# Performance work log

Hardware: AMD Instinct MI355X
Metric: run time of the kernel (lower is better)

## Reference

```python
import jax, jax.numpy as jnp
import numpy as np

NUM_QUBITS = 4
NUM_LAYERS = 3
B = 16384


def ry(t):
    # t: scalar or [B] -> [2,2] or [B,2,2] complex64
    c = jnp.cos(t / 2)
    s = jnp.sin(t / 2)
    return jnp.stack([jnp.stack([c, -s], -1), jnp.stack([s, c], -1)], -2).astype(jnp.complex64)


def rz(t):
    e = jnp.exp(-0.5j * t.astype(jnp.complex64))
    z = jnp.zeros_like(e)
    return jnp.stack([jnp.stack([e, z], -1), jnp.stack([z, jnp.conj(e)], -1)], -2)


def apply_gate(psi, G, wire):
    # psi: [B,2,2,2,2]; G: [2,2] (shared) or [B,2,2] (per-sample)
    ax = 1 + wire
    psi = jnp.moveaxis(psi, ax, -1)
    if G.ndim == 3:
        psi = jnp.einsum('b...j,bij->b...i', psi, G)
    else:
        psi = jnp.einsum('...j,ij->...i', psi, G)
    return jnp.moveaxis(psi, -1, ax)


def cnot(psi, c, t):
    ca, ta = 1 + c, 1 + t
    p0 = jnp.take(psi, 0, axis=ca)
    p1 = jnp.take(psi, 1, axis=ca)
    p1 = jnp.flip(p1, axis=ta - (1 if ta > ca else 0))
    return jnp.stack([p0, p1], axis=ca)


def quantum_layer(inputs, qw):
    # inputs: [B,4] angles; qw: [3,4,2] circuit weights -> [B,4] PauliZ expvals
    b = inputs.shape[0]
    psi = jnp.zeros((b, 2, 2, 2, 2), jnp.complex64).at[:, 0, 0, 0, 0].set(1.0)
    for w in range(NUM_QUBITS):
        psi = apply_gate(psi, ry(inputs[:, w]), w)
    for l in range(NUM_LAYERS):
        for q in range(NUM_QUBITS):
            psi = apply_gate(psi, ry(qw[l, q, 0]), q)
            psi = apply_gate(psi, rz(qw[l, q, 1]), q)
        for q in range(NUM_QUBITS - 1):
            psi = cnot(psi, q, q + 1)
        psi = cnot(psi, NUM_QUBITS - 1, 0)
    pr = jnp.real(psi * jnp.conj(psi))  # [B,2,2,2,2]
    signs = jnp.array([1.0, -1.0], jnp.float32)
    outs = []
    for w in range(NUM_QUBITS):
        shp = [1, 1, 1, 1, 1]
        shp[1 + w] = 2
        outs.append(jnp.sum(pr * signs.reshape(shp), axis=(1, 2, 3, 4)))
    return jnp.stack(outs, axis=1).astype(jnp.float32)


def setup_inputs() -> dict:
    key = jax.random.key(0)
    ks = jax.random.split(key, 10)
    x = jax.random.normal(ks[0], (B, 1280), jnp.float32)
    W1 = jax.random.normal(ks[1], (1280, 64), jnp.float32) * 0.03
    b1 = jnp.zeros((64,), jnp.float32)
    W2 = jax.random.normal(ks[2], (64, 4), jnp.float32) * 0.12
    b2 = jnp.zeros((4,), jnp.float32)
    qw = jax.random.normal(ks[3], (NUM_LAYERS, NUM_QUBITS, 2), jnp.float32) * 0.1
    Wc1 = jax.random.normal(ks[4], (8, 16), jnp.float32) * 0.35
    bc1 = jnp.zeros((16,), jnp.float32)
    Wc2 = jax.random.normal(ks[5], (16, 1), jnp.float32) * 0.25
    bc2 = jnp.zeros((1,), jnp.float32)
    return {"x": x, "W1": W1, "b1": b1, "W2": W2, "b2": b2, "qw": qw,
            "Wc1": Wc1, "bc1": bc1, "Wc2": Wc2, "bc2": bc2}


def reference(x, W1, b1, W2, b2, qw, Wc1, bc1, Wc2, bc2):
    # reducer: 1280 -> 64 -> 4 with tanh (dropout inactive in eval)
    h = jax.nn.relu(x @ W1 + b1)
    reduced = jnp.tanh(h @ W2 + b2)  # [B,4]
    quantum_out = quantum_layer(reduced, qw)  # [B,4]
    combined = jnp.concatenate([reduced, quantum_out], axis=1)  # [B,8]
    logits = jax.nn.relu(combined @ Wc1 + bc1) @ Wc2 + bc2  # [B,1]
    return logits
```

## Files before the change

kernel.cpp:

```cpp
#include <hip/hip_runtime.h>
#include <math.h>

typedef __attribute__((ext_vector_type(4))) float f32x4;
typedef __attribute__((ext_vector_type(8))) short s16x8;

__device__ __forceinline__ short f2bf_rne(float f) {
  unsigned u = __float_as_uint(f);
  unsigned r = u + 0x7FFFu + ((u >> 16) & 1u);
  return (short)(r >> 16);
}
__device__ __forceinline__ float bf2f(short b) {
  return __uint_as_float(((unsigned)(unsigned short)b) << 16);
}

#define WAIT_VMCNT(N) asm volatile("s_waitcnt vmcnt(" #N ")" ::: "memory")
#define BAR()         __builtin_amdgcn_s_barrier()
#define CFENCE()      asm volatile("" ::: "memory")
#define SCHEDB()      __builtin_amdgcn_sched_barrier(0)

__device__ __forceinline__ void gl_lds16(const void* g, void* l) {
  __builtin_amdgcn_global_load_lds(
      (const __attribute__((address_space(1))) void*)g,
      (__attribute__((address_space(3))) void*)l, 16, 0, 0);
}

#define GLOAD4(D, P) \
  asm volatile("global_load_dwordx4 %0, %1, off" : "=&v"(D) : "v"(P))

__global__ __launch_bounds__(256) void prep_w1(const float* __restrict__ W1,
                                               unsigned short* __restrict__ wf) {
  const int c   = blockIdx.x;
  const int l   = threadIdx.x & 63;
  const int nt  = threadIdx.x >> 6;
  const int kb  = c * 32 + (l >> 4) * 8;
  const int col = nt * 16 + (l & 15);
  s16x8 hi, lo;
#pragma unroll
  for (int j = 0; j < 8; ++j) {
    float f = W1[(kb + j) * 64 + col];
    short h = f2bf_rne(f);
    hi[j] = h;
    lo[j] = f2bf_rne(f - bf2f(h));
  }
  const int slot = (c * 4 + nt) * 2;
  *(s16x8*)(wf + (size_t)(slot * 64 + l) * 8)       = hi;
  *(s16x8*)(wf + (size_t)((slot + 1) * 64 + l) * 8) = lo;
}

#define APPLY_RY(BIT, C, S)                                                  \
  { _Pragma("unroll")                                                        \
    for (int i = 0; i < 16; ++i) {                                           \
      if (!(i & (BIT))) {                                                    \
        const int j = i | (BIT);                                             \
        float ar = re[i], ai = im[i], br = re[j], bi = im[j];                \
        re[i] = fmaf((C), ar, -(S) * br);                                    \
        im[i] = fmaf((C), ai, -(S) * bi);                                    \
        re[j] = fmaf((S), ar, (C) * br);                                     \
        im[j] = fmaf((S), ai, (C) * bi);                                     \
      }                                                                      \
    } }

#define APPLY_RZ(BIT, C, S)                                                  \
  { _Pragma("unroll")                                                        \
    for (int i = 0; i < 16; ++i) {                                           \
      float vr = re[i], vi = im[i];                                          \
      if (!(i & (BIT))) { re[i] = fmaf((C), vr, (S) * vi);                   \
                          im[i] = fmaf((C), vi, -(S) * vr); }                \
      else              { re[i] = fmaf((C), vr, -(S) * vi);                  \
                          im[i] = fmaf((C), vi, (S) * vr); }                 \
    } }

#define APPLY_CNOT(CB, TB)                                                   \
  { _Pragma("unroll")                                                        \
    for (int i = 0; i < 16; ++i) {                                           \
      if ((i & (CB)) && !(i & (TB))) {                                       \
        const int j = i | (TB);                                              \
        float t = re[i]; re[i] = re[j]; re[j] = t;                           \
        t = im[i]; im[i] = im[j]; im[j] = t;                                 \
      }                                                                      \
    } }

__device__ __forceinline__ float qfc_head(
    const float* __restrict__ red, const float* __restrict__ qw,
    const float* __restrict__ Wc1, const float* __restrict__ bc1,
    const float* __restrict__ Wc2, const float* __restrict__ bc2) {
  float re[16], im[16];
#pragma unroll
  for (int i = 0; i < 16; ++i) { re[i] = 0.f; im[i] = 0.f; }
  re[0] = 1.f;
  {
    float s0, c0; sincosf(0.5f * red[0], &s0, &c0); APPLY_RY(8, c0, s0);
    float s1, c1; sincosf(0.5f * red[1], &s1, &c1); APPLY_RY(4, c1, s1);
    float s2, c2; sincosf(0.5f * red[2], &s2, &c2); APPLY_RY(2, c2, s2);
    float s3, c3; sincosf(0.5f * red[3], &s3, &c3); APPLY_RY(1, c3, s3);
  }
  for (int lyr = 0; lyr < 3; ++lyr) {
    const float* ql = qw + lyr * 8;
    { float sn, cn; sincosf(0.5f * ql[0], &sn, &cn); APPLY_RY(8, cn, sn); }
    { float sn, cn; sincosf(0.5f * ql[1], &sn, &cn); APPLY_RZ(8, cn, sn); }
    { float sn, cn; sincosf(0.5f * ql[2], &sn, &cn); APPLY_RY(4, cn, sn); }
    { float sn, cn; sincosf(0.5f * ql[3], &sn, &cn); APPLY_RZ(4, cn, sn); }
    { float sn, cn; sincosf(0.5f * ql[4], &sn, &cn); APPLY_RY(2, cn, sn); }
    { float sn, cn; sincosf(0.5f * ql[5], &sn, &cn); APPLY_RZ(2, cn, sn); }
    { float sn, cn; sincosf(0.5f * ql[6], &sn, &cn); APPLY_RY(1, cn, sn); }
    { float sn, cn; sincosf(0.5f * ql[7], &sn, &cn); APPLY_RZ(1, cn, sn); }
    APPLY_CNOT(8, 4);
    APPLY_CNOT(4, 2);
    APPLY_CNOT(2, 1);
    APPLY_CNOT(1, 8);
  }
  float q0 = 0.f, q1 = 0.f, q2 = 0.f, q3 = 0.f;
#pragma unroll
  for (int i = 0; i < 16; ++i) {
    const float pr = fmaf(re[i], re[i], im[i] * im[i]);
    q0 += (i & 8) ? -pr : pr;
    q1 += (i & 4) ? -pr : pr;
    q2 += (i & 2) ? -pr : pr;
    q3 += (i & 1) ? -pr : pr;
  }
  float logit = bc2[0];
#pragma unroll
  for (int j = 0; j < 16; ++j) {
    float a = bc1[j];
    a = fmaf(red[0], Wc1[j],       a);
    a = fmaf(red[1], Wc1[16 + j],  a);
    a = fmaf(red[2], Wc1[32 + j],  a);
    a = fmaf(red[3], Wc1[48 + j],  a);
    a = fmaf(q0,     Wc1[64 + j],  a);
    a = fmaf(q1,     Wc1[80 + j],  a);
    a = fmaf(q2,     Wc1[96 + j],  a);
    a = fmaf(q3,     Wc1[112 + j], a);
    logit = fmaf(fmaxf(a, 0.f), Wc2[j], logit);
  }
  return logit;
}

__global__ __launch_bounds__(256) void qfc_gemm(
    const float* __restrict__ x,
    const unsigned short* __restrict__ wf,
    float* __restrict__ pw)
{
  __shared__ s16x8 Bs[3][512];

  const int tid  = threadIdx.x;
  const int l    = tid & 63;
  const int wv   = tid >> 6;
  const int bid  = blockIdx.x;
  const int rt   = bid / 5;
  const int kq   = bid - rt * 5;
  const int r0   = rt * 64;
  const int arow = l & 15;
  const int kg   = l >> 4;

  const float* xrow = x + (size_t)(r0 + wv * 16 + arow) * 1280 + kq * 256 + kg * 8;
  const s16x8* wfb = (const s16x8*)wf + (size_t)(kq * 8) * 512 + wv * 128 + l;

  f32x4 acc[4];
#pragma unroll
  for (int nt = 0; nt < 4; ++nt) acc[nt] = (f32x4)(0.f);

  float4 a00, a01, a10, a11, a20, a21;

  gl_lds16(wfb,      &Bs[0][wv * 128]);
  gl_lds16(wfb + 64, &Bs[0][wv * 128 + 64]);
  GLOAD4(a00, xrow);
  GLOAD4(a01, xrow + 4);
  gl_lds16(wfb + 512,      &Bs[1][wv * 128]);
  gl_lds16(wfb + 512 + 64, &Bs[1][wv * 128 + 64]);
  GLOAD4(a10, xrow + 32);
  GLOAD4(a11, xrow + 36);

#define CHUNK(C, AC0, AC1, AN0, AN1)                                          \
  {                                                                           \
    if ((C) < 7) { WAIT_VMCNT(4); } else { WAIT_VMCNT(0); }                   \
    BAR();                                                                    \
    CFENCE();                                                                 \
    SCHEDB();                                                                 \
    if ((C) + 2 < 8) {                                                        \
      const s16x8* bsrc_ = wfb + (size_t)((C) + 2) * 512;                     \
      gl_lds16(bsrc_,      &Bs[((C) + 2) % 3][wv * 128]);                     \
      gl_lds16(bsrc_ + 64, &Bs[((C) + 2) % 3][wv * 128 + 64]);                \
      GLOAD4(AN0, xrow + ((C) + 2) * 32);                                     \
      GLOAD4(AN1, xrow + ((C) + 2) * 32 + 4);                                 \
    }                                                                         \
    SCHEDB();                                                                 \
    float f_[8] = {AC0.x, AC0.y, AC0.z, AC0.w, AC1.x, AC1.y, AC1.z, AC1.w};   \
    s16x8 ah_, al_;                                                           \
    _Pragma("unroll")                                                         \
    for (int j = 0; j < 8; ++j) {                                             \
      short h_ = f2bf_rne(f_[j]);                                             \
      ah_[j] = h_;                                                            \
      al_[j] = (short)(__float_as_uint(f_[j] - bf2f(h_)) >> 16);              \
    }                                                                         \
    _Pragma("unroll")                                                         \
    for (int nt = 0; nt < 4; ++nt) {                                          \
      s16x8 bh_ = Bs[(C) % 3][(nt * 2) * 64 + l];                             \
      s16x8 bl_ = Bs[(C) % 3][(nt * 2 + 1) * 64 + l];                         \
      acc[nt] = __builtin_amdgcn_mfma_f32_16x16x32_bf16(ah_, bh_, acc[nt], 0, 0, 0); \
      acc[nt] = __builtin_amdgcn_mfma_f32_16x16x32_bf16(al_, bh_, acc[nt], 0, 0, 0); \
      acc[nt] = __builtin_amdgcn_mfma_f32_16x16x32_bf16(ah_, bl_, acc[nt], 0, 0, 0); \
    }                                                                         \
  }

  CHUNK(0, a00, a01, a20, a21)
  CHUNK(1, a10, a11, a00, a01)
  CHUNK(2, a20, a21, a10, a11)
  CHUNK(3, a00, a01, a20, a21)
  CHUNK(4, a10, a11, a00, a01)
  CHUNK(5, a20, a21, a10, a11)
  CHUNK(6, a00, a01, a20, a21)
  CHUNK(7, a10, a11, a00, a01)
#undef CHUNK

  float* wsp = pw + (size_t)bid * 4096;
#pragma unroll
  for (int nt = 0; nt < 4; ++nt)
    *(float4*)(wsp + (nt * 16 + arow) * 64 + wv * 16 + kg * 4) =
        make_float4(acc[nt][0], acc[nt][1], acc[nt][2], acc[nt][3]);
}

__global__ __launch_bounds__(256) void qfc_tail(
    const float* __restrict__ pw,
    const float* __restrict__ b1, const float* __restrict__ W2,
    const float* __restrict__ b2, const float* __restrict__ qw,
    const float* __restrict__ Wc1, const float* __restrict__ bc1,
    const float* __restrict__ Wc2, const float* __restrict__ bc2,
    float* __restrict__ out) {
  const int tid = threadIdx.x;
  const int s   = tid >> 2;
  const int cq  = tid & 3;
  const int rt  = blockIdx.x;
  const float* pb = pw + (size_t)rt * 5 * 4096;

  float h4[4] = {0.f, 0.f, 0.f, 0.f};
#pragma unroll
  for (int cc = 0; cc < 16; ++cc) {
    const int c = cq * 16 + cc;
    const int o = c * 64 + s;
    float p = pb[o];
#pragma unroll
    for (int q = 1; q < 5; ++q) p += pb[q * 4096 + o];
    float hv = fmaxf(p + b1[c], 0.f);
    const float4 w2 = *(const float4*)(W2 + c * 4);
    h4[0] = fmaf(hv, w2.x, h4[0]);
    h4[1] = fmaf(hv, w2.y, h4[1]);
    h4[2] = fmaf(hv, w2.z, h4[2]);
    h4[3] = fmaf(hv, w2.w, h4[3]);
  }
#pragma unroll
  for (int k = 0; k < 4; ++k) {
    h4[k] += __shfl_xor(h4[k], 1);
    h4[k] += __shfl_xor(h4[k], 2);
  }

  float red[4];
#pragma unroll
  for (int k = 0; k < 4; ++k) red[k] = tanhf(h4[k] + b2[k]);

  const float logit = qfc_head(red, qw, Wc1, bc1, Wc2, bc2);
  if (cq == 0) out[rt * 64 + s] = logit;
}

#define NKT 20
__global__ __launch_bounds__(256) void qfc_fused(
    const float* __restrict__ x, const float* __restrict__ W1,
    const float* __restrict__ b1, const float* __restrict__ W2,
    const float* __restrict__ b2, const float* __restrict__ qw,
    const float* __restrict__ Wc1, const float* __restrict__ bc1,
    const float* __restrict__ Wc2, const float* __restrict__ bc2,
    float* __restrict__ out) {
  __shared__ float lds[16384];
  const int tid = threadIdx.x;
  const int lane = tid & 63;
  const int wv = tid >> 6;
  const int rg = lane >> 3;
  const int cg = lane & 7;
  const int r0 = blockIdx.x * 64;
  float acc[8][8];
#pragma unroll
  for (int i = 0; i < 8; ++i)
#pragma unroll
    for (int j = 0; j < 8; ++j) acc[i][j] = 0.f;
  const float* xrow = x + (size_t)(r0 + lane) * 1280 + wv * 16;
  const int aBase = wv * 1024;
  const int bBase = 8192 + wv * 1024;
  float4 a_st[4], b_st[4];
  auto issue_loads = [&](int kt) {
    const float* ap = xrow + kt * 64;
#pragma unroll
    for (int i = 0; i < 4; ++i) a_st[i] = *(const float4*)(ap + i * 4);
    const float* bp = W1 + kt * 4096 + wv * 1024 + lane * 4;
#pragma unroll
    for (int i = 0; i < 4; ++i) b_st[i] = *(const float4*)(bp + i * 256);
  };
  auto write_stage = [&](int buf) {
    float* A = &lds[buf * 4096 + aBase];
#pragma unroll
    for (int i = 0; i < 4; ++i) {
      float* p = A + i * 256 + lane;
      p[0] = a_st[i].x; p[64] = a_st[i].y; p[128] = a_st[i].z; p[192] = a_st[i].w;
    }
    float* Bp = &lds[buf * 4096 + bBase + lane * 4];
#pragma unroll
    for (int i = 0; i < 4; ++i) *(float4*)(Bp + i * 256) = b_st[i];
  };
  auto compute_tile = [&](int buf) {
#pragma unroll
    for (int m = 0; m < 16; ++m) {
      const float* Ak = &lds[buf * 4096 + aBase + m * 64];
      const float* Bk = &lds[buf * 4096 + bBase + m * 64];
      const float4 a0 = *(const float4*)(Ak + rg * 8);
      const float4 a1 = *(const float4*)(Ak + rg * 8 + 4);
      const float4 c0 = *(const float4*)(Bk + cg * 8);
      const float4 c1 = *(const float4*)(Bk + cg * 8 + 4);
      const float av[8] = {a0.x, a0.y, a0.z, a0.w, a1.x, a1.y, a1.z, a1.w};
      const float bv[8] = {c0.x, c0.y, c0.z, c0.w, c1.x, c1.y, c1.z, c1.w};
#pragma unroll
      for (int i = 0; i < 8; ++i)
#pragma unroll
        for (int j = 0; j < 8; ++j) acc[i][j] = fmaf(av[i], bv[j], acc[i][j]);
    }
  };
  issue_loads(0);
  write_stage(0);
  for (int kt = 0; kt < NKT; ++kt) {
    const int buf = kt & 1;
    if (kt + 1 < NKT) issue_loads(kt + 1);
    compute_tile(buf);
    if (kt + 1 < NKT) write_stage(buf ^ 1);
  }
  __syncthreads();
#pragma unroll
  for (int j = 0; j < 8; ++j) {
    const int c = cg * 8 + j;
    float* p = &lds[wv * 4096 + c * 64 + rg * 8];
    *(float4*)p = make_float4(acc[0][j], acc[1][j], acc[2][j], acc[3][j]);
    *(float4*)(p + 4) = make_float4(acc[4][j], acc[5][j], acc[6][j], acc[7][j]);
  }
  __syncthreads();
  const int s = tid >> 2;
  const int cq = tid & 3;
  float h4[4] = {0.f, 0.f, 0.f, 0.f};
#pragma unroll
  for (int cc = 0; cc < 16; ++cc) {
    const int c = cq * 16 + cc;
    const int o = c * 64 + s;
    float pp = (lds[o] + lds[4096 + o]) + (lds[8192 + o] + lds[12288 + o]);
    float hv = fmaxf(pp + b1[c], 0.f);
    const float4 w2 = *(const float4*)(W2 + c * 4);
    h4[0] = fmaf(hv, w2.x, h4[0]);
    h4[1] = fmaf(hv, w2.y, h4[1]);
    h4[2] = fmaf(hv, w2.z, h4[2]);
    h4[3] = fmaf(hv, w2.w, h4[3]);
  }
#pragma unroll
  for (int k = 0; k < 4; ++k) {
    h4[k] += __shfl_xor(h4[k], 1);
    h4[k] += __shfl_xor(h4[k], 2);
  }
  float red[4];
#pragma unroll
  for (int k = 0; k < 4; ++k) red[k] = tanhf(h4[k] + b2[k]);
  const float logit = qfc_head(red, qw, Wc1, bc1, Wc2, bc2);
  if (cq == 0) out[r0 + s] = logit;
}

extern "C" void kernel_launch(void* const* d_in, const int* in_sizes, int n_in,
                              void* d_out, int out_size, void* d_ws, size_t ws_size,
                              hipStream_t stream) {
  const float* x   = (const float*)d_in[0];
  const float* W1  = (const float*)d_in[1];
  const float* b1  = (const float*)d_in[2];
  const float* W2  = (const float*)d_in[3];
  const float* b2  = (const float*)d_in[4];
  const float* qw  = (const float*)d_in[5];
  const float* Wc1 = (const float*)d_in[6];
  const float* bc1 = (const float*)d_in[7];
  const float* Wc2 = (const float*)d_in[8];
  const float* bc2 = (const float*)d_in[9];

  const size_t WF_BYTES = 327680;
  const size_t PW_OFF   = WF_BYTES;
  const size_t PW_BYTES = (size_t)1280 * 4096 * 4;
  if (ws_size >= PW_OFF + PW_BYTES) {
    unsigned short* wf = (unsigned short*)d_ws;
    float* pw = (float*)((char*)d_ws + PW_OFF);
    prep_w1<<<dim3(40), dim3(256), 0, stream>>>(W1, wf);
    qfc_gemm<<<dim3(1280), dim3(256), 0, stream>>>(x, wf, pw);
    qfc_tail<<<dim3(256), dim3(256), 0, stream>>>(
        pw, b1, W2, b2, qw, Wc1, bc1, Wc2, bc2, (float*)d_out);
  } else {
    qfc_fused<<<dim3(256), dim3(256), 0, stream>>>(
        x, W1, b1, W2, b2, qw, Wc1, bc1, Wc2, bc2, (float*)d_out);
  }
}
```

Before: 40.39 us.

## Deepen GEMM prefetch to four stages, remap blocks by k-slice, use nontemporal x loads

The split-K GEMM pipeline moves from triple to quadruple buffering, so A and W1 chunks are prefetched three steps ahead with adjusted vmcnt waits. Block IDs are remapped so groups of row tiles sharing the same K slice run together, which should improve L2 reuse of the weight slice, and the workspace index is recomputed to match. The streaming x loads get the nt hint to avoid polluting cache. In exchange the kernel uses more LDS and registers, which could lower occupancy.

```diff
diff --git a/kernel.cpp b/kernel.cpp
--- a/kernel.cpp
+++ b/kernel.cpp
@@ -24,8 +24,8 @@
       (__attribute__((address_space(3))) void*)l, 16, 0, 0);
 }
 
-#define GLOAD4(D, P) \
-  asm volatile("global_load_dwordx4 %0, %1, off" : "=&v"(D) : "v"(P))
+#define GLOAD4NT(D, P) \
+  asm volatile("global_load_dwordx4 %0, %1, off nt" : "=&v"(D) : "v"(P))
 
 __global__ __launch_bounds__(256) void prep_w1(const float* __restrict__ W1,
                                                unsigned short* __restrict__ wf) {
@@ -140,14 +140,15 @@
     const unsigned short* __restrict__ wf,
     float* __restrict__ pw)
 {
-  __shared__ s16x8 Bs[3][512];
+  __shared__ s16x8 Bs[4][512];
 
   const int tid  = threadIdx.x;
   const int l    = tid & 63;
   const int wv   = tid >> 6;
   const int bid  = blockIdx.x;
-  const int rt   = bid / 5;
-  const int kq   = bid - rt * 5;
+  const int s_   = bid >> 3;
+  const int kq   = s_ >> 5;
+  const int rt   = (bid & 7) + ((s_ & 31) << 3);
   const int r0   = rt * 64;
   const int arow = l & 15;
   const int kg   = l >> 4;
@@ -159,29 +160,35 @@
 #pragma unroll
   for (int nt = 0; nt < 4; ++nt) acc[nt] = (f32x4)(0.f);
 
-  float4 a00, a01, a10, a11, a20, a21;
-
-  gl_lds16(wfb,      &Bs[0][wv * 128]);
-  gl_lds16(wfb + 64, &Bs[0][wv * 128 + 64]);
-  GLOAD4(a00, xrow);
-  GLOAD4(a01, xrow + 4);
-  gl_lds16(wfb + 512,      &Bs[1][wv * 128]);
-  gl_lds16(wfb + 512 + 64, &Bs[1][wv * 128 + 64]);
-  GLOAD4(a10, xrow + 32);
-  GLOAD4(a11, xrow + 36);
+  float4 a00, a01, a10, a11, a20, a21, a30, a31;
+
+  gl_lds16(wfb,             &Bs[0][wv * 128]);
+  gl_lds16(wfb + 64,        &Bs[0][wv * 128 + 64]);
+  GLOAD4NT(a00, xrow);
+  GLOAD4NT(a01, xrow + 4);
+  gl_lds16(wfb + 512,       &Bs[1][wv * 128]);
+  gl_lds16(wfb + 512 + 64,  &Bs[1][wv * 128 + 64]);
+  GLOAD4NT(a10, xrow + 32);
+  GLOAD4NT(a11, xrow + 36);
+  gl_lds16(wfb + 1024,      &Bs[2][wv * 128]);
+  gl_lds16(wfb + 1024 + 64, &Bs[2][wv * 128 + 64]);
+  GLOAD4NT(a20, xrow + 64);
+  GLOAD4NT(a21, xrow + 68);
 
 #define CHUNK(C, AC0, AC1, AN0, AN1)                                          \
   {                                                                           \
-    if ((C) < 7) { WAIT_VMCNT(4); } else { WAIT_VMCNT(0); }                   \
+    if ((C) <= 5) { WAIT_VMCNT(8); }                                          \
+    else if ((C) == 6) { WAIT_VMCNT(4); }                                     \
+    else { WAIT_VMCNT(0); }                                                   \
     BAR();                                                                    \
     CFENCE();                                                                 \
     SCHEDB();                                                                 \
-    if ((C) + 2 < 8) {                                                        \
-      const s16x8* bsrc_ = wfb + (size_t)((C) + 2) * 512;                     \
-      gl_lds16(bsrc_,      &Bs[((C) + 2) % 3][wv * 128]);                     \
-      gl_lds16(bsrc_ + 64, &Bs[((C) + 2) % 3][wv * 128 + 64]);                \
-      GLOAD4(AN0, xrow + ((C) + 2) * 32);                                     \
-      GLOAD4(AN1, xrow + ((C) + 2) * 32 + 4);                                 \
+    if ((C) + 3 < 8) {                                                        \
+      const s16x8* bsrc_ = wfb + (size_t)((C) + 3) * 512;                     \
+      gl_lds16(bsrc_,      &Bs[((C) + 3) & 3][wv * 128]);                     \
+      gl_lds16(bsrc_ + 64, &Bs[((C) + 3) & 3][wv * 128 + 64]);                \
+      GLOAD4NT(AN0, xrow + ((C) + 3) * 32);                                   \
+      GLOAD4NT(AN1, xrow + ((C) + 3) * 32 + 4);                               \
     }                                                                         \
     SCHEDB();                                                                 \
     float f_[8] = {AC0.x, AC0.y, AC0.z, AC0.w, AC1.x, AC1.y, AC1.z, AC1.w};   \
@@ -194,25 +201,25 @@
     }                                                                         \
     _Pragma("unroll")                                                         \
     for (int nt = 0; nt < 4; ++nt) {                                          \
-      s16x8 bh_ = Bs[(C) % 3][(nt * 2) * 64 + l];                             \
-      s16x8 bl_ = Bs[(C) % 3][(nt * 2 + 1) * 64 + l];                         \
+      s16x8 bh_ = Bs[(C) & 3][(nt * 2) * 64 + l];                             \
+      s16x8 bl_ = Bs[(C) & 3][(nt * 2 + 1) * 64 + l];                         \
       acc[nt] = __builtin_amdgcn_mfma_f32_16x16x32_bf16(ah_, bh_, acc[nt], 0, 0, 0); \
       acc[nt] = __builtin_amdgcn_mfma_f32_16x16x32_bf16(al_, bh_, acc[nt], 0, 0, 0); \
       acc[nt] = __builtin_amdgcn_mfma_f32_16x16x32_bf16(ah_, bl_, acc[nt], 0, 0, 0); \
     }                                                                         \
   }
 
-  CHUNK(0, a00, a01, a20, a21)
+  CHUNK(0, a00, a01, a30, a31)
   CHUNK(1, a10, a11, a00, a01)
   CHUNK(2, a20, a21, a10, a11)
-  CHUNK(3, a00, a01, a20, a21)
-  CHUNK(4, a10, a11, a00, a01)
-  CHUNK(5, a20, a21, a10, a11)
-  CHUNK(6, a00, a01, a20, a21)
-  CHUNK(7, a10, a11, a00, a01)
+  CHUNK(3, a30, a31, a20, a21)
+  CHUNK(4, a00, a01, a30, a31)
+  CHUNK(5, a10, a11, a00, a01)
+  CHUNK(6, a20, a21, a10, a11)
+  CHUNK(7, a30, a31, a00, a01)
 #undef CHUNK
 
-  float* wsp = pw + (size_t)bid * 4096;
+  float* wsp = pw + (size_t)(rt * 5 + kq) * 4096;
 #pragma unroll
   for (int nt = 0; nt < 4; ++nt)
     *(float4*)(wsp + (nt * 16 + arow) * 64 + wv * 16 + kg * 4) =
```

Measured after the change: 52.67 us. 30.4% more time.

## Fuse split-K GEMM and tail into one kernel with per-wave K slices

Applied to the files above, without the earlier changes.

Replaces the split-K GEMM plus separate tail kernel with a single kernel. Each block handles 16 rows, and each of its four waves covers a quarter of K. B fragments are loaded straight into registers with a deeper prefetch instead of being staged through LDS with barriers. Partial sums are reduced in LDS and the MLP/quantum head runs in the same block, which removes the large global partial-sum workspace round trip and one launch. The cost is that each wave now reads all 64 columns of W1 from global or L2 without sharing them across waves, and the tail runs on only one wave per block.

```diff
diff --git a/kernel.cpp b/kernel.cpp
--- a/kernel.cpp
+++ b/kernel.cpp
@@ -14,15 +14,7 @@
 }
 
 #define WAIT_VMCNT(N) asm volatile("s_waitcnt vmcnt(" #N ")" ::: "memory")
-#define BAR()         __builtin_amdgcn_s_barrier()
-#define CFENCE()      asm volatile("" ::: "memory")
 #define SCHEDB()      __builtin_amdgcn_sched_barrier(0)
-
-__device__ __forceinline__ void gl_lds16(const void* g, void* l) {
-  __builtin_amdgcn_global_load_lds(
-      (const __attribute__((address_space(1))) void*)g,
-      (__attribute__((address_space(3))) void*)l, 16, 0, 0);
-}
 
 #define GLOAD4(D, P) \
   asm volatile("global_load_dwordx4 %0, %1, off" : "=&v"(D) : "v"(P))
@@ -135,56 +127,51 @@
   return logit;
 }
 
-__global__ __launch_bounds__(256) void qfc_gemm(
+__global__ __launch_bounds__(256) void qfc_pinned(
     const float* __restrict__ x,
     const unsigned short* __restrict__ wf,
-    float* __restrict__ pw)
-{
-  __shared__ s16x8 Bs[3][512];
-
-  const int tid  = threadIdx.x;
-  const int l    = tid & 63;
-  const int wv   = tid >> 6;
-  const int bid  = blockIdx.x;
-  const int rt   = bid / 5;
-  const int kq   = bid - rt * 5;
-  const int r0   = rt * 64;
-  const int arow = l & 15;
-  const int kg   = l >> 4;
-
-  const float* xrow = x + (size_t)(r0 + wv * 16 + arow) * 1280 + kq * 256 + kg * 8;
-  const s16x8* wfb = (const s16x8*)wf + (size_t)(kq * 8) * 512 + wv * 128 + l;
+    const float* __restrict__ b1, const float* __restrict__ W2,
+    const float* __restrict__ b2, const float* __restrict__ qw,
+    const float* __restrict__ Wc1, const float* __restrict__ bc1,
+    const float* __restrict__ Wc2, const float* __restrict__ bc2,
+    float* __restrict__ out) {
+  __shared__ float lds[4096];
+
+  const int tid   = threadIdx.x;
+  const int l     = tid & 63;
+  const int wv    = tid >> 6;
+  const int rbase = blockIdx.x * 16;
+  const int arow  = l & 15;
+  const int kg    = l >> 4;
+
+  const float* xp = x + (size_t)(rbase + arow) * 1280 + wv * 320 + kg * 8;
+  const s16x8* bw = (const s16x8*)wf + (size_t)wv * 5120 + l;
 
   f32x4 acc[4];
 #pragma unroll
   for (int nt = 0; nt < 4; ++nt) acc[nt] = (f32x4)(0.f);
 
-  float4 a00, a01, a10, a11, a20, a21;
-
-  gl_lds16(wfb,      &Bs[0][wv * 128]);
-  gl_lds16(wfb + 64, &Bs[0][wv * 128 + 64]);
-  GLOAD4(a00, xrow);
-  GLOAD4(a01, xrow + 4);
-  gl_lds16(wfb + 512,      &Bs[1][wv * 128]);
-  gl_lds16(wfb + 512 + 64, &Bs[1][wv * 128 + 64]);
-  GLOAD4(a10, xrow + 32);
-  GLOAD4(a11, xrow + 36);
-
-#define CHUNK(C, AC0, AC1, AN0, AN1)                                          \
+  f32x4 apf[4][2];
+  s16x8 bpf[2][8];
+
+#define ISSUE_A(SLOT, C)                       \
+  { GLOAD4(apf[SLOT][0], xp + (C) * 32);       \
+    GLOAD4(apf[SLOT][1], xp + (C) * 32 + 4); }
+#define ISSUE_B(SLOT, C)                                   \
+  { _Pragma("unroll")                                      \
+    for (int q_ = 0; q_ < 8; ++q_)                         \
+      GLOAD4(bpf[SLOT][q_], bw + (C) * 512 + q_ * 64); }
+
+  ISSUE_A(0, 0) ISSUE_A(1, 1) ISSUE_A(2, 2) ISSUE_A(3, 3)
+  ISSUE_B(0, 0) ISSUE_B(1, 1)
+
+#define CHUNK(C, WN, IA, IB)                                                  \
   {                                                                           \
-    if ((C) < 7) { WAIT_VMCNT(4); } else { WAIT_VMCNT(0); }                   \
-    BAR();                                                                    \
-    CFENCE();                                                                 \
+    WAIT_VMCNT(WN);                                                           \
     SCHEDB();                                                                 \
-    if ((C) + 2 < 8) {                                                        \
-      const s16x8* bsrc_ = wfb + (size_t)((C) + 2) * 512;                     \
-      gl_lds16(bsrc_,      &Bs[((C) + 2) % 3][wv * 128]);                     \
-      gl_lds16(bsrc_ + 64, &Bs[((C) + 2) % 3][wv * 128 + 64]);                \
-      GLOAD4(AN0, xrow + ((C) + 2) * 32);                                     \
-      GLOAD4(AN1, xrow + ((C) + 2) * 32 + 4);                                 \
-    }                                                                         \
-    SCHEDB();                                                                 \
-    float f_[8] = {AC0.x, AC0.y, AC0.z, AC0.w, AC1.x, AC1.y, AC1.z, AC1.w};   \
+    float f_[8] = {apf[(C) & 3][0].x, apf[(C) & 3][0].y, apf[(C) & 3][0].z,   \
+                   apf[(C) & 3][0].w, apf[(C) & 3][1].x, apf[(C) & 3][1].y,   \
+                   apf[(C) & 3][1].z, apf[(C) & 3][1].w};                     \
     s16x8 ah_, al_;                                                           \
     _Pragma("unroll")                                                         \
     for (int j = 0; j < 8; ++j) {                                             \
@@ -194,71 +181,65 @@
     }                                                                         \
     _Pragma("unroll")                                                         \
     for (int nt = 0; nt < 4; ++nt) {                                          \
-      s16x8 bh_ = Bs[(C) % 3][(nt * 2) * 64 + l];                             \
-      s16x8 bl_ = Bs[(C) % 3][(nt * 2 + 1) * 64 + l];                         \
-      acc[nt] = __builtin_amdgcn_mfma_f32_16x16x32_bf16(ah_, bh_, acc[nt], 0, 0, 0); \
-      acc[nt] = __builtin_amdgcn_mfma_f32_16x16x32_bf16(al_, bh_, acc[nt], 0, 0, 0); \
-      acc[nt] = __builtin_amdgcn_mfma_f32_16x16x32_bf16(ah_, bl_, acc[nt], 0, 0, 0); \
+      acc[nt] = __builtin_amdgcn_mfma_f32_16x16x32_bf16(ah_, bpf[(C) & 1][nt * 2],     acc[nt], 0, 0, 0); \
+      acc[nt] = __builtin_amdgcn_mfma_f32_16x16x32_bf16(al_, bpf[(C) & 1][nt * 2],     acc[nt], 0, 0, 0); \
+      acc[nt] = __builtin_amdgcn_mfma_f32_16x16x32_bf16(ah_, bpf[(C) & 1][nt * 2 + 1], acc[nt], 0, 0, 0); \
     }                                                                         \
-  }
-
-  CHUNK(0, a00, a01, a20, a21)
-  CHUNK(1, a10, a11, a00, a01)
-  CHUNK(2, a20, a21, a10, a11)
-  CHUNK(3, a00, a01, a20, a21)
-  CHUNK(4, a10, a11, a00, a01)
-  CHUNK(5, a20, a21, a10, a11)
-  CHUNK(6, a00, a01, a20, a21)
-  CHUNK(7, a10, a11, a00, a01)
+    SCHEDB();                                                                 \
+    if (IA) ISSUE_A((C) & 3, (C) + 4)                                         \
+    if (IB) ISSUE_B((C) & 1, (C) + 2)                                         \
+  }
+
+  CHUNK(0, 8,  1, 1)
+  CHUNK(1, 10, 1, 1)
+  CHUNK(2, 10, 1, 1)
+  CHUNK(3, 10, 1, 1)
+  CHUNK(4, 10, 1, 1)
+  CHUNK(5, 10, 1, 1)
+  CHUNK(6, 10, 0, 1)
+  CHUNK(7, 8,  0, 1)
+  CHUNK(8, 8,  0, 0)
+  CHUNK(9, 0,  0, 0)
 #undef CHUNK
-
-  float* wsp = pw + (size_t)bid * 4096;
+#undef ISSUE_A
+#undef ISSUE_B
+
 #pragma unroll
   for (int nt = 0; nt < 4; ++nt)
-    *(float4*)(wsp + (nt * 16 + arow) * 64 + wv * 16 + kg * 4) =
+    *(float4*)&lds[wv * 1024 + (nt * 16 + arow) * 16 + kg * 4] =
         make_float4(acc[nt][0], acc[nt][1], acc[nt][2], acc[nt][3]);
-}
-
-__global__ __launch_bounds__(256) void qfc_tail(
-    const float* __restrict__ pw,
-    const float* __restrict__ b1, const float* __restrict__ W2,
-    const float* __restrict__ b2, const float* __restrict__ qw,
-    const float* __restrict__ Wc1, const float* __restrict__ bc1,
-    const float* __restrict__ Wc2, const float* __restrict__ bc2,
-    float* __restrict__ out) {
-  const int tid = threadIdx.x;
-  const int s   = tid >> 2;
-  const int cq  = tid & 3;
-  const int rt  = blockIdx.x;
-  const float* pb = pw + (size_t)rt * 5 * 4096;
-
-  float h4[4] = {0.f, 0.f, 0.f, 0.f};
-#pragma unroll
-  for (int cc = 0; cc < 16; ++cc) {
-    const int c = cq * 16 + cc;
-    const int o = c * 64 + s;
-    float p = pb[o];
-#pragma unroll
-    for (int q = 1; q < 5; ++q) p += pb[q * 4096 + o];
-    float hv = fmaxf(p + b1[c], 0.f);
-    const float4 w2 = *(const float4*)(W2 + c * 4);
-    h4[0] = fmaf(hv, w2.x, h4[0]);
-    h4[1] = fmaf(hv, w2.y, h4[1]);
-    h4[2] = fmaf(hv, w2.z, h4[2]);
-    h4[3] = fmaf(hv, w2.w, h4[3]);
-  }
-#pragma unroll
-  for (int k = 0; k < 4; ++k) {
-    h4[k] += __shfl_xor(h4[k], 1);
-    h4[k] += __shfl_xor(h4[k], 2);
-  }
-
-  float red[4];
-#pragma unroll
-  for (int k = 0; k < 4; ++k) red[k] = tanhf(h4[k] + b2[k]);
-
-  const float logit = qfc_head(red, qw, Wc1, bc1, Wc2, bc2);
-  if (cq == 0) out[rt * 64 + s] = logit;
+  __syncthreads();
+
+  if (tid < 64) {
+    const int s  = tid >> 2;
+    const int cq = tid & 3;
+
+    float h4[4] = {0.f, 0.f, 0.f, 0.f};
+#pragma unroll
+    for (int cc = 0; cc < 16; ++cc) {
+      const int c = cq * 16 + cc;
+      const int o = c * 16 + s;
+      float p  = (lds[o] + lds[1024 + o]) + (lds[2048 + o] + lds[3072 + o]);
+      float hv = fmaxf(p + b1[c], 0.f);
+      const float4 w2 = *(const float4*)(W2 + c * 4);
+      h4[0] = fmaf(hv, w2.x, h4[0]);
+      h4[1] = fmaf(hv, w2.y, h4[1]);
+      h4[2] = fmaf(hv, w2.z, h4[2]);
+      h4[3] = fmaf(hv, w2.w, h4[3]);
+    }
+#pragma unroll
+    for (int k = 0; k < 4; ++k) {
+      h4[k] += __shfl_xor(h4[k], 1);
+      h4[k] += __shfl_xor(h4[k], 2);
+    }
+
+    float red[4];
+#pragma unroll
+    for (int k = 0; k < 4; ++k) red[k] = tanhf(h4[k] + b2[k]);
+
+    const float logit = qfc_head(red, qw, Wc1, bc1, Wc2, bc2);
+    if (cq == 0) out[rbase + s] = logit;
+  }
 }
 
 #define NKT 20
@@ -380,15 +361,11 @@
   const float* bc2 = (const float*)d_in[9];
 
   const size_t WF_BYTES = 327680;
-  const size_t PW_OFF   = WF_BYTES;
-  const size_t PW_BYTES = (size_t)1280 * 4096 * 4;
-  if (ws_size >= PW_OFF + PW_BYTES) {
+  if (ws_size >= WF_BYTES) {
     unsigned short* wf = (unsigned short*)d_ws;
-    float* pw = (float*)((char*)d_ws + PW_OFF);
     prep_w1<<<dim3(40), dim3(256), 0, stream>>>(W1, wf);
-    qfc_gemm<<<dim3(1280), dim3(256), 0, stream>>>(x, wf, pw);
-    qfc_tail<<<dim3(256), dim3(256), 0, stream>>>(
-        pw, b1, W2, b2, qw, Wc1, bc1, Wc2, bc2, (float*)d_out);
+    qfc_pinned<<<dim3(1024), dim3(256), 0, stream>>>(
+        x, wf, b1, W2, b2, qw, Wc1, bc1, Wc2, bc2, (float*)d_out);
   } else {
     qfc_fused<<<dim3(256), dim3(256), 0, stream>>>(
         x, W1, b1, W2, b2, qw, Wc1, bc1, Wc2, bc2, (float*)d_out);
```

Measured after the change: 40.33 us. About the same (-0.2%).
